# Kernel tuning notes

Measured on AMD Instinct MI355X. Metric: run time of the kernel, lower is better.

Reference implementation:

```python
import jax, jax.numpy as jnp
import numpy as np
import math

EMBED_DIM = 2048
NUM_HEADS = 16
HEAD_DIM = EMBED_DIM // NUM_HEADS
BATCH = 2
SEQ = 2048


def setup_inputs() -> dict:
    key = jax.random.key(0)
    ks = jax.random.split(key, 6)
    x = jax.random.normal(ks[0], (BATCH, SEQ, EMBED_DIM), dtype=jnp.float32)
    # causal mask: True = masked (upper triangle, strictly above diagonal)
    attn_mask = jnp.triu(jnp.ones((SEQ, SEQ), dtype=bool), k=1)
    s = 1.0 / math.sqrt(EMBED_DIM)
    W_qkv = jax.random.normal(ks[1], (3 * EMBED_DIM, EMBED_DIM), dtype=jnp.float32) * s
    b_qkv = jax.random.normal(ks[2], (3 * EMBED_DIM,), dtype=jnp.float32) * 0.01
    W_out = jax.random.normal(ks[3], (EMBED_DIM, EMBED_DIM), dtype=jnp.float32) * s
    b_out = jax.random.normal(ks[4], (EMBED_DIM,), dtype=jnp.float32) * 0.01
    return {"x": x, "W_qkv": W_qkv, "b_qkv": b_qkv, "W_out": W_out,
            "b_out": b_out, "attn_mask": attn_mask}


def reference(x, W_qkv, b_qkv, W_out, b_out, attn_mask):
    B, S, E = x.shape
    # fused QKV projection: [B,S,3E]
    qkv = jnp.einsum('bse,fe->bsf', x, W_qkv) + b_qkv
    qkv = qkv.reshape(B, S, 3, NUM_HEADS, HEAD_DIM)
    qkv = jnp.transpose(qkv, (2, 0, 3, 1, 4))  # [3,B,H,S,Dh]
    q, k, v = qkv[0], qkv[1], qkv[2]
    scale = 1.0 / math.sqrt(HEAD_DIM)
    scores = jnp.einsum('bhqd,bhkd->bhqk', q, k) * scale  # [B,H,S,S]
    scores = jnp.where(attn_mask[None, None, :, :], -jnp.inf, scores)
    attn = jax.nn.softmax(scores, axis=-1)
    out = jnp.einsum('bhqk,bhkd->bhqd', attn, v)  # [B,H,S,Dh]
    out = jnp.transpose(out, (0, 2, 1, 3)).reshape(B, S, E)
    out = jnp.einsum('bse,fe->bsf', out, W_out) + b_out
    return out
```

## Files before the change

### kernel.cpp

```cpp
#include <hip/hip_runtime.h>
#include <hip/hip_bf16.h>
#include <math.h>

#define SEQ   2048
#define EMBED 2048
#define NHEAD 16
#define DHEAD 128
#define BATCH 2

#define NX   ((size_t)BATCH * SEQ * EMBED)
#define NW1  ((size_t)3 * EMBED * EMBED)
#define NB1  ((size_t)3 * EMBED)
#define NW2  ((size_t)EMBED * EMBED)
#define NB2  ((size_t)EMBED)

typedef __bf16 bf16;
typedef __attribute__((__ext_vector_type__(8))) __bf16 bf16x8;
typedef __attribute__((__ext_vector_type__(4))) __bf16 bf16x4;
typedef __attribute__((__ext_vector_type__(4))) float f32x4;
typedef __attribute__((__ext_vector_type__(4))) unsigned int u32x4;

#define NEG_BIG (-1.0e30f)

__device__ __forceinline__ f32x4 mfma_16x16x32(bf16x8 a, bf16x8 b, f32x4 c) {
  return __builtin_amdgcn_mfma_f32_16x16x32_bf16(a, b, c, 0, 0, 0);
}

__device__ __forceinline__ void llds16(bf16* dst, const bf16* src) {
  __builtin_amdgcn_global_load_lds(
      (const __attribute__((address_space(1))) void*)src,
      (__attribute__((address_space(3))) void*)dst, 16, 0, 0);
}

__global__ void convert_inputs(const void* __restrict__ xin,
                               const void* __restrict__ w1in,
                               const void* __restrict__ b1in,
                               const void* __restrict__ w2in,
                               const void* __restrict__ b2in,
                               bf16* __restrict__ xb, bf16* __restrict__ w1b,
                               bf16* __restrict__ b1b, bf16* __restrict__ w2b,
                               bf16* __restrict__ b2b, int* __restrict__ flagp)
{
  __shared__ int sflag;
  if (threadIdx.x == 0) sflag = 0;
  __syncthreads();
  const unsigned short* xh = (const unsigned short*)xin;
  int huge = 0;
  for (int i = threadIdx.x; i < 2048; i += 256) {
    float f = __uint_as_float((unsigned int)xh[i] << 16);
    if (!(fabsf(f) <= 1e4f)) huge = 1;
  }
  if (huge) sflag = 1;
  __syncthreads();
  const int isf32 = sflag;
  if (blockIdx.x == 0 && threadIdx.x == 0) *flagp = isf32;

  const void* srcs[5] = {xin, w1in, b1in, w2in, b2in};
  bf16* dsts[5] = {xb, w1b, b1b, w2b, b2b};
  const size_t lens[5] = {NX, NW1, NB1, NW2, NB2};
  const size_t gid = (size_t)blockIdx.x * blockDim.x + threadIdx.x;
  const size_t gstride = (size_t)gridDim.x * blockDim.x;
  for (int sidx = 0; sidx < 5; ++sidx) {
    const size_t n8 = lens[sidx] >> 3;
    bf16* d = dsts[sidx];
    if (isf32) {
      const float* s = (const float*)srcs[sidx];
      for (size_t i = gid; i < n8; i += gstride) {
        const float* sp = s + i * 8;
        bf16x8 r;
#pragma unroll
        for (int j = 0; j < 8; ++j) r[j] = (bf16)sp[j];
        *(bf16x8*)(d + i * 8) = r;
      }
    } else {
      const u32x4* s = (const u32x4*)srcs[sidx];
      for (size_t i = gid; i < n8; i += gstride)
        *(u32x4*)(d + i * 8) = s[i];
    }
  }
}

template <int MODE>
__global__ __launch_bounds__(256, 4) void gemm_nt(
    const bf16* __restrict__ A, const bf16* __restrict__ B,
    const bf16* __restrict__ bias, int K,
    void* __restrict__ out0v, bf16* __restrict__ out1, bf16* __restrict__ out2,
    const int* __restrict__ flagp)
{
  __shared__ bf16 sA[128 * 32];
  __shared__ bf16 sB[128 * 32];
  const int t = threadIdx.x;
  const int lane = t & 63, w = t >> 6;
  const int wm = w >> 1, wn = w & 1;
  const int lr = lane & 15, lq = lane >> 4;
  const int m0 = blockIdx.y * 128, n0 = blockIdx.x * 128;

  f32x4 acc[4][4];
#pragma unroll
  for (int i = 0; i < 4; ++i)
#pragma unroll
    for (int j = 0; j < 4; ++j) acc[i][j] = (f32x4){0.f, 0.f, 0.f, 0.f};

  const bf16* Abase = A + (size_t)m0 * K;
  const bf16* Bbase = B + (size_t)n0 * K;
  const int nK = K >> 5;
  for (int kk = 0; kk < nK; ++kk) {
    const int k0 = kk << 5;
    __syncthreads();
#pragma unroll
    for (int i = 0; i < 2; ++i) {
      const int c = i * 256 + t;
      const int ldsbase = (i * 256 + (t & ~63)) << 3;
      llds16(sA + ldsbase, Abase + (size_t)(c >> 2) * K + k0 + (c & 3) * 8);
      llds16(sB + ldsbase, Bbase + (size_t)(c >> 2) * K + k0 + (c & 3) * 8);
    }
    __syncthreads();

    bf16x8 af[4], bfr[4];
#pragma unroll
    for (int mi = 0; mi < 4; ++mi)
      af[mi] = *(const bf16x8*)(sA + (wm * 64 + mi * 16 + lr) * 32 + lq * 8);
#pragma unroll
    for (int ni = 0; ni < 4; ++ni)
      bfr[ni] = *(const bf16x8*)(sB + (wn * 64 + ni * 16 + lr) * 32 + lq * 8);
#pragma unroll
    for (int mi = 0; mi < 4; ++mi)
#pragma unroll
      for (int ni = 0; ni < 4; ++ni)
        acc[mi][ni] = mfma_16x16x32(af[mi], bfr[ni], acc[mi][ni]);
  }

  if (MODE == 0) {
    const int which = n0 >> 11;
    const int h = (n0 >> 7) & 15;
    const int bb = m0 >> 11;
    const int s0 = m0 & 2047;
    if (which == 2) {
      bf16* dst = out2;
#pragma unroll
      for (int ni = 0; ni < 4; ++ni) {
        const int col = wn * 64 + ni * 16 + lr;
        const float bv = (float)bias[n0 + col];
        bf16* rowp = dst + ((size_t)(bb * NHEAD + h) * DHEAD + col) * SEQ + s0;
#pragma unroll
        for (int mi = 0; mi < 4; ++mi) {
          bf16x4 pk;
#pragma unroll
          for (int reg = 0; reg < 4; ++reg)
            pk[reg] = (bf16)(acc[mi][ni][reg] + bv);
          *(bf16x4*)(rowp + wm * 64 + mi * 16 + lq * 4) = pk;
        }
      }
    } else {
      bf16* dst = (which == 0) ? (bf16*)out0v : out1;
#pragma unroll
      for (int ni = 0; ni < 4; ++ni) {
        const int col = wn * 64 + ni * 16 + lr;
        const float bv = (float)bias[n0 + col];
#pragma unroll
        for (int mi = 0; mi < 4; ++mi)
#pragma unroll
          for (int reg = 0; reg < 4; ++reg) {
            const int row = wm * 64 + mi * 16 + lq * 4 + reg;
            const int s = s0 + row;
            dst[((size_t)(bb * NHEAD + h) * SEQ + s) * DHEAD + col] =
                (bf16)(acc[mi][ni][reg] + bv);
          }
      }
    }
  } else {
    const int isf32 = *flagp;
#pragma unroll
    for (int ni = 0; ni < 4; ++ni) {
      const int col = wn * 64 + ni * 16 + lr;
      const float bv = (float)bias[n0 + col];
#pragma unroll
      for (int mi = 0; mi < 4; ++mi)
#pragma unroll
        for (int reg = 0; reg < 4; ++reg) {
          const int row = wm * 64 + mi * 16 + lq * 4 + reg;
          const float v = acc[mi][ni][reg] + bv;
          const size_t idx = (size_t)(m0 + row) * EMBED + n0 + col;
          if (isf32) ((float*)out0v)[idx] = v;
          else       ((bf16*)out0v)[idx] = (bf16)v;
        }
    }
  }
}

__device__ __forceinline__ void qk_softmax_tile(
    const bf16* __restrict__ sK, bf16* __restrict__ sP, const bf16x8* aq,
    float* m_i, float* l_i, f32x4* oacc, int kt, int qt,
    int w, int lr, int lq, int sPofs)
{
  const float scale = 0.08838834764831845f;
  f32x4 sacc[4];
#pragma unroll
  for (int ni = 0; ni < 4; ++ni) sacc[ni] = (f32x4){0.f, 0.f, 0.f, 0.f};
#pragma unroll
  for (int ks = 0; ks < 4; ++ks)
#pragma unroll
    for (int ni = 0; ni < 4; ++ni) {
      bf16x8 bk = *(const bf16x8*)(sK + (ni * 16 + lr) * 136 + ks * 32 + lq * 8);
      sacc[ni] = mfma_16x16x32(aq[ks], bk, sacc[ni]);
    }
  float pp[4][4];
#pragma unroll
  for (int ni = 0; ni < 4; ++ni)
#pragma unroll
    for (int reg = 0; reg < 4; ++reg) {
      float sv = sacc[ni][reg] * scale;
      if (kt == qt) {
        const int kg = kt * 64 + ni * 16 + lr;
        const int qg = qt * 64 + w * 16 + lq * 4 + reg;
        if (kg > qg) sv = NEG_BIG;
      }
      pp[ni][reg] = sv;
    }
#pragma unroll
  for (int reg = 0; reg < 4; ++reg) {
    float mx = fmaxf(fmaxf(pp[0][reg], pp[1][reg]), fmaxf(pp[2][reg], pp[3][reg]));
#pragma unroll
    for (int off = 1; off < 16; off <<= 1)
      mx = fmaxf(mx, __shfl_xor(mx, off, 64));
    const float mnew = fmaxf(m_i[reg], mx);
    const float alpha = __expf(m_i[reg] - mnew);
    float ls = 0.f;
#pragma unroll
    for (int ni = 0; ni < 4; ++ni) {
      pp[ni][reg] = __expf(pp[ni][reg] - mnew);
      ls += pp[ni][reg];
    }
#pragma unroll
    for (int off = 1; off < 16; off <<= 1) ls += __shfl_xor(ls, off, 64);
    l_i[reg] = l_i[reg] * alpha + ls;
    m_i[reg] = mnew;
#pragma unroll
    for (int dt = 0; dt < 8; ++dt) oacc[dt][reg] *= alpha;
  }
#pragma unroll
  for (int ni = 0; ni < 4; ++ni)
#pragma unroll
    for (int reg = 0; reg < 4; ++reg)
      sP[(sPofs + w * 16 + lq * 4 + reg) * 72 + ni * 16 + lr] =
          (bf16)pp[ni][reg];
}

__device__ __forceinline__ void pv_tile(const bf16* __restrict__ sP,
                                        const bf16* __restrict__ sV,
                                        f32x4* oacc, int w, int lr, int lq,
                                        int sPofs)
{
#pragma unroll
  for (int ks2 = 0; ks2 < 2; ++ks2) {
    bf16x8 ap =
        *(const bf16x8*)(sP + (sPofs + w * 16 + lr) * 72 + ks2 * 32 + lq * 8);
#pragma unroll
    for (int dt = 0; dt < 8; ++dt) {
      bf16x8 bv =
          *(const bf16x8*)(sV + (dt * 16 + lr) * 72 + ks2 * 32 + lq * 8);
      oacc[dt] = mfma_16x16x32(ap, bv, oacc[dt]);
    }
  }
}

__global__ __launch_bounds__(256, 2) void attn_fwd(
    const bf16* __restrict__ qb, const bf16* __restrict__ kb,
    const bf16* __restrict__ vt, bf16* __restrict__ aout)
{
  __shared__ bf16 sK[64 * 136];
  __shared__ bf16 sV[128 * 72];
  __shared__ bf16 sP[128 * 72];
  const int t = threadIdx.x;
  const int lane = t & 63, w = t >> 6;
  const int lr = lane & 15, lq = lane >> 4;
  const int p  = blockIdx.x & 15;
  const int bh = blockIdx.x >> 4;
  const int bb = bh >> 4, h = bh & 15;
  const int qlo = p, qhi = 31 - p;

  bf16x8 aqL[4], aqH[4];
  {
    const bf16* qpL =
        qb + ((size_t)bh * SEQ + qlo * 64 + w * 16 + lr) * DHEAD + lq * 8;
    const bf16* qpH =
        qb + ((size_t)bh * SEQ + qhi * 64 + w * 16 + lr) * DHEAD + lq * 8;
#pragma unroll
    for (int ks = 0; ks < 4; ++ks) {
      aqL[ks] = *(const bf16x8*)(qpL + ks * 32);
      aqH[ks] = *(const bf16x8*)(qpH + ks * 32);
    }
  }

  f32x4 oL[8], oH[8];
#pragma unroll
  for (int i = 0; i < 8; ++i) {
    oL[i] = (f32x4){0.f, 0.f, 0.f, 0.f};
    oH[i] = (f32x4){0.f, 0.f, 0.f, 0.f};
  }
  float mL[4] = {NEG_BIG, NEG_BIG, NEG_BIG, NEG_BIG};
  float mH[4] = {NEG_BIG, NEG_BIG, NEG_BIG, NEG_BIG};
  float lL[4] = {0.f, 0.f, 0.f, 0.f};
  float lH[4] = {0.f, 0.f, 0.f, 0.f};

  bf16x8 rk[4], rv[4];
  const int kr_ = t >> 4, kd_ = t & 15;
  const int vr_ = t >> 3, vk_ = t & 7;
#define FETCH(ktv)                                                          \
  {                                                                         \
    const int _kt = (ktv);                                                  \
    _Pragma("unroll") for (int i = 0; i < 4; ++i) {                         \
      rk[i] = *(const bf16x8*)(kb + ((size_t)bh * SEQ + _kt * 64 +          \
                                     (i * 16 + kr_)) * DHEAD + kd_ * 8);    \
      rv[i] = *(const bf16x8*)(vt + ((size_t)bh * DHEAD + (i * 32 + vr_)) * \
                                     SEQ + _kt * 64 + vk_ * 8);             \
    }                                                                       \
  }
#define COMMIT()                                                            \
  {                                                                         \
    _Pragma("unroll") for (int i = 0; i < 4; ++i) {                         \
      *(bf16x8*)(sK + (i * 16 + kr_) * 136 + kd_ * 8) = rk[i];              \
      *(bf16x8*)(sV + (i * 32 + vr_) * 72 + vk_ * 8) = rv[i];               \
    }                                                                       \
  }

  FETCH(0);
  COMMIT();
  __syncthreads();

  for (int kt = 0; kt <= qhi; ++kt) {
    if (kt < qhi) FETCH(kt + 1);
    const bool doLo = (kt <= qlo);

    qk_softmax_tile(sK, sP, aqH, mH, lH, oH, kt, qhi, w, lr, lq, 64);
    if (doLo) qk_softmax_tile(sK, sP, aqL, mL, lL, oL, kt, qlo, w, lr, lq, 0);
    asm volatile("s_waitcnt lgkmcnt(0)" ::: "memory");
    pv_tile(sP, sV, oH, w, lr, lq, 64);
    if (doLo) pv_tile(sP, sV, oL, w, lr, lq, 0);

    __syncthreads();
    if (kt < qhi) {
      COMMIT();
      __syncthreads();
    }
  }

#pragma unroll
  for (int side = 0; side < 2; ++side) {
    const f32x4* oacc = side ? oH : oL;
    const float* l_i = side ? lH : lL;
    const int qt = side ? qhi : qlo;
    float inv[4];
#pragma unroll
    for (int reg = 0; reg < 4; ++reg) inv[reg] = 1.0f / l_i[reg];
#pragma unroll
    for (int dt = 0; dt < 8; ++dt)
#pragma unroll
      for (int reg = 0; reg < 4; ++reg) {
        const int qg = qt * 64 + w * 16 + lq * 4 + reg;
        aout[((size_t)bb * SEQ + qg) * EMBED + h * 128 + dt * 16 + lr] =
            (bf16)(oacc[dt][reg] * inv[reg]);
      }
  }
#undef FETCH
#undef COMMIT
}

extern "C" void kernel_launch(void* const* d_in, const int* in_sizes, int n_in,
                              void* d_out, int out_size, void* d_ws, size_t ws_size,
                              hipStream_t stream) {
  const void* x    = d_in[0];
  const void* Wqkv = d_in[1];
  const void* bqkv = d_in[2];
  const void* Wout = d_in[3];
  const void* bout = d_in[4];

  int* flagp = (int*)d_ws;
  bf16* base = (bf16*)((char*)d_ws + 256);
  bf16* xb   = base;
  bf16* w1b  = xb + NX;
  bf16* b1b  = w1b + NW1;
  bf16* w2b  = b1b + NB1;
  bf16* b2b  = w2b + NW2;
  bf16* qb   = b2b + NB2;
  bf16* kb   = qb + NX;
  bf16* vt   = kb + NX;
  bf16* aout = vt + NX;

  dim3 blk(256);
  convert_inputs<<<dim3(1024), blk, 0, stream>>>(
      x, Wqkv, bqkv, Wout, bout, xb, w1b, b1b, w2b, b2b, flagp);
  gemm_nt<0><<<dim3(48, 32), blk, 0, stream>>>(xb, w1b, b1b, EMBED,
                                               (void*)qb, kb, vt, flagp);
  attn_fwd<<<dim3(512), blk, 0, stream>>>(qb, kb, vt, aout);
  gemm_nt<1><<<dim3(16, 32), blk, 0, stream>>>(aout, w2b, b2b, EMBED,
                                               d_out, nullptr, nullptr, flagp);
}
```

Before: 472.3 us.

## Transpose attention MFMA orientation so each lane owns one query row

Swaps the MFMA operand order for both QK^T and PV so the accumulator layout puts one query row per lane column. Row max and sum reductions drop from four 4-step shuffles to two shuffles, and per-row softmax state becomes scalar. P is written to LDS as packed bf16x4 with an XOR swizzle instead of a padded stride, and the output is stored as bf16x4 vectors. The aim is less shuffle and VALU work and fewer scalar LDS and global stores, at the cost of swizzled indexing complexity.

Measured after the change: 409.7 us. -13.2%, faster.

```diff
diff --git a/kernel.cpp b/kernel.cpp
--- a/kernel.cpp
+++ b/kernel.cpp
@@ -190,60 +190,74 @@
 
 __device__ __forceinline__ void qk_softmax_tile(
     const bf16* __restrict__ sK, bf16* __restrict__ sP, const bf16x8* aq,
-    float* m_i, float* l_i, f32x4* oacc, int kt, int qt,
+    float& m_i, float& l_i, f32x4* oacc, int kt, int qt,
     int w, int lr, int lq, int sPofs)
 {
   const float scale = 0.08838834764831845f;
-  f32x4 sacc[4];
-#pragma unroll
-  for (int ni = 0; ni < 4; ++ni) sacc[ni] = (f32x4){0.f, 0.f, 0.f, 0.f};
+  f32x4 tacc[4];
+#pragma unroll
+  for (int ni = 0; ni < 4; ++ni) tacc[ni] = (f32x4){0.f, 0.f, 0.f, 0.f};
 #pragma unroll
   for (int ks = 0; ks < 4; ++ks)
 #pragma unroll
     for (int ni = 0; ni < 4; ++ni) {
       bf16x8 bk = *(const bf16x8*)(sK + (ni * 16 + lr) * 136 + ks * 32 + lq * 8);
-      sacc[ni] = mfma_16x16x32(aq[ks], bk, sacc[ni]);
+      tacc[ni] = mfma_16x16x32(bk, aq[ks], tacc[ni]);
     }
   float pp[4][4];
+  const int qg = qt * 64 + w * 16 + lr;
 #pragma unroll
   for (int ni = 0; ni < 4; ++ni)
 #pragma unroll
     for (int reg = 0; reg < 4; ++reg) {
-      float sv = sacc[ni][reg] * scale;
+      float sv = tacc[ni][reg] * scale;
       if (kt == qt) {
-        const int kg = kt * 64 + ni * 16 + lr;
-        const int qg = qt * 64 + w * 16 + lq * 4 + reg;
+        const int kg = kt * 64 + ni * 16 + lq * 4 + reg;
         if (kg > qg) sv = NEG_BIG;
       }
       pp[ni][reg] = sv;
     }
-#pragma unroll
-  for (int reg = 0; reg < 4; ++reg) {
-    float mx = fmaxf(fmaxf(pp[0][reg], pp[1][reg]), fmaxf(pp[2][reg], pp[3][reg]));
-#pragma unroll
-    for (int off = 1; off < 16; off <<= 1)
-      mx = fmaxf(mx, __shfl_xor(mx, off, 64));
-    const float mnew = fmaxf(m_i[reg], mx);
-    const float alpha = __expf(m_i[reg] - mnew);
-    float ls = 0.f;
-#pragma unroll
-    for (int ni = 0; ni < 4; ++ni) {
-      pp[ni][reg] = __expf(pp[ni][reg] - mnew);
-      ls += pp[ni][reg];
-    }
-#pragma unroll
-    for (int off = 1; off < 16; off <<= 1) ls += __shfl_xor(ls, off, 64);
-    l_i[reg] = l_i[reg] * alpha + ls;
-    m_i[reg] = mnew;
-#pragma unroll
-    for (int dt = 0; dt < 8; ++dt) oacc[dt][reg] *= alpha;
-  }
-#pragma unroll
-  for (int ni = 0; ni < 4; ++ni)
-#pragma unroll
-    for (int reg = 0; reg < 4; ++reg)
-      sP[(sPofs + w * 16 + lq * 4 + reg) * 72 + ni * 16 + lr] =
-          (bf16)pp[ni][reg];
+  float m01, m23, mx;
+  {
+    float a0 = fmaxf(fmaxf(pp[0][0], pp[0][1]), fmaxf(pp[0][2], pp[0][3]));
+    float a1 = fmaxf(fmaxf(pp[1][0], pp[1][1]), fmaxf(pp[1][2], pp[1][3]));
+    float a2 = fmaxf(fmaxf(pp[2][0], pp[2][1]), fmaxf(pp[2][2], pp[2][3]));
+    float a3 = fmaxf(fmaxf(pp[3][0], pp[3][1]), fmaxf(pp[3][2], pp[3][3]));
+    m01 = fmaxf(a0, a1);
+    m23 = fmaxf(a2, a3);
+    mx = fmaxf(m01, m23);
+  }
+  mx = fmaxf(mx, __shfl_xor(mx, 16, 64));
+  mx = fmaxf(mx, __shfl_xor(mx, 32, 64));
+  const float mnew = fmaxf(m_i, mx);
+  const float alpha = __expf(m_i - mnew);
+  float ls = 0.f;
+#pragma unroll
+  for (int ni = 0; ni < 4; ++ni) {
+    float s0 = __expf(pp[ni][0] - mnew);
+    float s1 = __expf(pp[ni][1] - mnew);
+    float s2 = __expf(pp[ni][2] - mnew);
+    float s3 = __expf(pp[ni][3] - mnew);
+    pp[ni][0] = s0; pp[ni][1] = s1; pp[ni][2] = s2; pp[ni][3] = s3;
+    ls += (s0 + s1) + (s2 + s3);
+  }
+  ls += __shfl_xor(ls, 16, 64);
+  ls += __shfl_xor(ls, 32, 64);
+  l_i = l_i * alpha + ls;
+  m_i = mnew;
+#pragma unroll
+  for (int dt = 0; dt < 8; ++dt) oacc[dt] *= alpha;
+  bf16* rowp = sP + (sPofs + w * 16 + lr) * 64;
+  const int swz = lr & 7;
+#pragma unroll
+  for (int ni = 0; ni < 4; ++ni) {
+    bf16x4 pk;
+#pragma unroll
+    for (int reg = 0; reg < 4; ++reg) pk[reg] = (bf16)pp[ni][reg];
+    const int col = ni * 16 + lq * 4;
+    const int scol = (((col >> 3) ^ swz) << 3) | (col & 7);
+    *(bf16x4*)(rowp + scol) = pk;
+  }
 }
 
 __device__ __forceinline__ void pv_tile(const bf16* __restrict__ sP,
@@ -251,15 +265,17 @@
                                         f32x4* oacc, int w, int lr, int lq,
                                         int sPofs)
 {
+  const bf16* rowp = sP + (sPofs + w * 16 + lr) * 64;
+  const int swz = lr & 7;
 #pragma unroll
   for (int ks2 = 0; ks2 < 2; ++ks2) {
-    bf16x8 ap =
-        *(const bf16x8*)(sP + (sPofs + w * 16 + lr) * 72 + ks2 * 32 + lq * 8);
+    const int chunk = ks2 * 4 + lq;
+    bf16x8 bp = *(const bf16x8*)(rowp + ((chunk ^ swz) << 3));
 #pragma unroll
     for (int dt = 0; dt < 8; ++dt) {
-      bf16x8 bv =
+      bf16x8 av =
           *(const bf16x8*)(sV + (dt * 16 + lr) * 72 + ks2 * 32 + lq * 8);
-      oacc[dt] = mfma_16x16x32(ap, bv, oacc[dt]);
+      oacc[dt] = mfma_16x16x32(av, bp, oacc[dt]);
     }
   }
 }
@@ -270,7 +286,7 @@
 {
   __shared__ bf16 sK[64 * 136];
   __shared__ bf16 sV[128 * 72];
-  __shared__ bf16 sP[128 * 72];
+  __shared__ bf16 sP[128 * 64];
   const int t = threadIdx.x;
   const int lane = t & 63, w = t >> 6;
   const int lr = lane & 15, lq = lane >> 4;
@@ -298,10 +314,8 @@
     oL[i] = (f32x4){0.f, 0.f, 0.f, 0.f};
     oH[i] = (f32x4){0.f, 0.f, 0.f, 0.f};
   }
-  float mL[4] = {NEG_BIG, NEG_BIG, NEG_BIG, NEG_BIG};
-  float mH[4] = {NEG_BIG, NEG_BIG, NEG_BIG, NEG_BIG};
-  float lL[4] = {0.f, 0.f, 0.f, 0.f};
-  float lH[4] = {0.f, 0.f, 0.f, 0.f};
+  float mL = NEG_BIG, mH = NEG_BIG;
+  float lL = 0.f, lH = 0.f;
 
   bf16x8 rk[4], rv[4];
   const int kr_ = t >> 4, kd_ = t & 15;
@@ -348,19 +362,18 @@
 #pragma unroll
   for (int side = 0; side < 2; ++side) {
     const f32x4* oacc = side ? oH : oL;
-    const float* l_i = side ? lH : lL;
+    const float linv = 1.0f / (side ? lH : lL);
     const int qt = side ? qhi : qlo;
-    float inv[4];
-#pragma unroll
-    for (int reg = 0; reg < 4; ++reg) inv[reg] = 1.0f / l_i[reg];
-#pragma unroll
-    for (int dt = 0; dt < 8; ++dt)
-#pragma unroll
-      for (int reg = 0; reg < 4; ++reg) {
-        const int qg = qt * 64 + w * 16 + lq * 4 + reg;
-        aout[((size_t)bb * SEQ + qg) * EMBED + h * 128 + dt * 16 + lr] =
-            (bf16)(oacc[dt][reg] * inv[reg]);
-      }
+    const int qg = qt * 64 + w * 16 + lr;
+    bf16* outp = aout + ((size_t)bb * SEQ + qg) * EMBED + h * 128 + lq * 4;
+#pragma unroll
+    for (int dt = 0; dt < 8; ++dt) {
+      bf16x4 pk;
+#pragma unroll
+      for (int reg = 0; reg < 4; ++reg)
+        pk[reg] = (bf16)(oacc[dt][reg] * linv);
+      *(bf16x4*)(outp + dt * 16) = pk;
+    }
   }
 #undef FETCH
 #undef COMMIT
```
